# Optimization experiments

Measured on AMD Instinct MI355X. Metric: run time of the kernel, lower is better.

## Reference

```python
import jax, jax.numpy as jnp
import numpy as np

EPS = 0.001
WEIGHT = 1.0


def _grid_sample_zeros(x, grid):
    """Bilinear grid_sample, align_corners=True, zeros padding.
    x: [B,C,H,W], grid: [B,H,W,2] in [-1,1] (x then y). Returns [B,C,H,W]."""
    B, C, H, W = x.shape
    gx = (grid[..., 0] + 1.0) * 0.5 * (W - 1)  # [B,H,W] pixel coords
    gy = (grid[..., 1] + 1.0) * 0.5 * (H - 1)
    x0 = jnp.floor(gx)
    y0 = jnp.floor(gy)
    x1 = x0 + 1.0
    y1 = y0 + 1.0
    wx1 = gx - x0
    wx0 = 1.0 - wx1
    wy1 = gy - y0
    wy0 = 1.0 - wy1

    def corner(xi, yi, w):
        valid = ((xi >= 0) & (xi <= W - 1) & (yi >= 0) & (yi <= H - 1)).astype(x.dtype)
        xc = jnp.clip(xi.astype(jnp.int32), 0, W - 1)
        yc = jnp.clip(yi.astype(jnp.int32), 0, H - 1)
        vals = jax.vmap(lambda img, yy, xx: img[:, yy, xx])(x, yc, xc)  # [B,C,H,W]
        return vals * (w * valid)[:, None, :, :]

    return (corner(x0, y0, wx0 * wy0) + corner(x1, y0, wx1 * wy0)
            + corner(x0, y1, wx0 * wy1) + corner(x1, y1, wx1 * wy1))


def _warp(x, flo):
    """Warp x by flow flo (pixel units), with validity mask. x,flo: [B,*,H,W]."""
    B, C, H, W = x.shape
    xx = jnp.arange(W, dtype=x.dtype)[None, :]  # [1,W]
    yy = jnp.arange(H, dtype=x.dtype)[:, None]  # [H,1]
    grid = jnp.stack([jnp.broadcast_to(xx, (H, W)), jnp.broadcast_to(yy, (H, W))], 0)  # [2,H,W]
    vgrid = grid[None] + flo  # [B,2,H,W]
    vx = 2.0 * vgrid[:, 0] / max(W - 1, 1) - 1.0
    vy = 2.0 * vgrid[:, 1] / max(H - 1, 1) - 1.0
    vgrid_n = jnp.stack([vx, vy], -1)  # [B,H,W,2]
    out = _grid_sample_zeros(x, vgrid_n)
    ones = jnp.ones_like(x)
    mask = _grid_sample_zeros(ones, vgrid_n)
    mask = jnp.where(mask < 0.9999, 0.0, 1.0).astype(x.dtype)
    mask = jax.lax.stop_gradient(mask)  # torch writes constants in-place -> no grad
    return out * mask


def setup_inputs() -> dict:
    key = jax.random.key(0)
    k1, k2 = jax.random.split(key)
    N, H, W = 16, 768, 768
    UV_AtoB = jax.random.normal(k1, (N, 2, H, W), dtype=jnp.float32)
    UV_BtoA = jax.random.normal(k2, (N, 2, H, W), dtype=jnp.float32)
    return {"UV_AtoB": UV_AtoB, "UV_BtoA": UV_BtoA}


def reference(UV_AtoB, UV_BtoA):
    N, C, H, W = UV_AtoB.shape
    xx = jnp.broadcast_to(jnp.arange(W, dtype=jnp.float32)[None, :], (H, W))
    yy = jnp.broadcast_to(jnp.arange(H, dtype=jnp.float32)[:, None], (H, W))
    GridXY = jnp.stack([xx / max(W - 1, 1), yy / max(H - 1, 1)], 0)  # [2,H,W]
    GridXY = jnp.broadcast_to(GridXY[None], (N, 2, H, W))

    def cycle_loss(flo1, flo2):
        m = _warp(GridXY, flo1)
        m = _warp(m, flo2)
        diff = jnp.sqrt(jnp.sum((GridXY - m) ** 2, axis=1) + EPS ** 2)  # [N,H,W]
        per = jnp.sum(diff, axis=(1, 2)) / (H * W)
        return jnp.sum(per) / N

    totloss_ABA = cycle_loss(UV_AtoB, UV_BtoA)
    totloss_BAB = cycle_loss(UV_BtoA, UV_AtoB)
    return (totloss_BAB + totloss_ABA) * WEIGHT
```

## Files before the change

kernel.cpp:

```cpp
#include <hip/hip_runtime.h>

constexpr int N = 16, H = 768, W = 768;
constexpr int HW = H * W;
constexpr float EPS2 = 1.0e-6f;
constexpr float INV_W1 = 1.0f / (float)(W - 1);
constexpr float INV_H1 = 1.0f / (float)(H - 1);
constexpr float WM1 = (float)(W - 1);
constexpr float HM1 = (float)(H - 1);
constexpr float WM2 = (float)(W - 2);

constexpr int TILE_COLS = 80;
constexpr int TILE_ROWS = 24;
constexpr int C_HALO = 8;
constexpr int R_HALO = 4;
constexpr int LSTRIDE = TILE_COLS;
constexpr int TILE_FLOATS = TILE_ROWS * LSTRIDE * 2;
constexpr int NBLK_X = W / 64, NBLK_Y = H / 16;
constexpr int NBLOCKS = NBLK_X * NBLK_Y * N;

typedef float float2a __attribute__((ext_vector_type(2), aligned(4)));

struct DirMeta { float gx, gy; int xb, y0, y1; };

__device__ __forceinline__ void dir_meta(float fx, float fy, int x, int y, DirMeta& m) {
    m.gx = (float)x + fx;
    m.gy = (float)y + fy;
    float x0f = floorf(m.gx);
    float y0f = floorf(m.gy);
    m.xb = (int)fminf(fmaxf(x0f, 0.0f), WM2);
    m.y0 = (int)fminf(fmaxf(y0f, 0.0f), HM1);
    m.y1 = (int)fminf(fmaxf(y0f + 1.0f, 0.0f), HM1);
}

__device__ __forceinline__ bool fast_ok(const DirMeta& m,
                                        float2a g0, float2a g1, float2a g2, float2a g3) {
    float x0f = floorf(m.gx), y0f = floorf(m.gy);
    bool ok = (x0f >= 0.0f) & (x0f <= WM2) & (y0f >= 0.0f) & (y0f <= HM1 - 1.0f);
    float x1f = x0f + 1.0f, y1f = y0f + 1.0f;
    float gx00 = x0f + g0.x, gx01 = x1f + g0.y;
    float gx10 = x0f + g2.x, gx11 = x1f + g2.y;
    float gy00 = y0f + g1.x, gy01 = y0f + g1.y;
    float gy10 = y1f + g3.x, gy11 = y1f + g3.y;
    float xlo = fminf(fminf(gx00, gx01), fminf(gx10, gx11));
    float xhi = fmaxf(fmaxf(gx00, gx01), fmaxf(gx10, gx11));
    float ylo = fminf(fminf(gy00, gy01), fminf(gy10, gy11));
    float yhi = fmaxf(fmaxf(gy00, gy01), fmaxf(gy10, gy11));
    ok &= (xlo >= 0.0f) & (xhi <= WM1) & (ylo >= 0.0f) & (yhi <= HM1);
    return ok;
}

__device__ __forceinline__ float fast_eval(const DirMeta& m,
                                           float2a g0, float2a g1, float2a g2, float2a g3,
                                           float fxc, float fyc) {
    float x0f = floorf(m.gx), y0f = floorf(m.gy);
    float wx1 = m.gx - x0f, wy1 = m.gy - y0f;
    float ftx = fmaf(wx1, g0.y - g0.x, g0.x);
    float fbx = fmaf(wx1, g2.y - g2.x, g2.x);
    float fxv = fmaf(wy1, fbx - ftx, ftx);
    float fty = fmaf(wx1, g1.y - g1.x, g1.x);
    float fby = fmaf(wx1, g3.y - g3.x, g3.x);
    float fyv = fmaf(wy1, fby - fty, fty);
    float a = (fxc + fxv) * INV_W1;
    float b = (fyc + fyv) * INV_H1;
    return sqrtf(fmaf(a, a, fmaf(b, b, EPS2)));
}

__device__ __forceinline__ float2 wg(float fx, float fy, float xi, float yi) {
    float gx = xi + fx, gy = yi + fy;
    float x0 = floorf(gx), y0 = floorf(gy);
    float wx1 = gx - x0, wx0 = 1.0f - wx1;
    float wy1 = gy - y0, wy0 = 1.0f - wy1;
    float vx0 = (x0 >= 0.0f  && x0 <= WM1)        ? 1.0f : 0.0f;
    float vx1 = (x0 >= -1.0f && x0 <= WM1 - 1.0f) ? 1.0f : 0.0f;
    float vy0 = (y0 >= 0.0f  && y0 <= HM1)        ? 1.0f : 0.0f;
    float vy1 = (y0 >= -1.0f && y0 <= HM1 - 1.0f) ? 1.0f : 0.0f;
    float ax = wx0 * vx0, bx = wx1 * vx1, sx = ax + bx;
    float ay = wy0 * vy0, by = wy1 * vy1, sy = ay + by;
    float ms = sx * sy;
    float kx = (ms >= 0.9999f) ? INV_W1 : 0.0f;
    float ky = (ms >= 0.9999f) ? INV_H1 : 0.0f;
    float2 r;
    r.x = fmaf(sx, x0, bx) * sy * kx;
    r.y = fmaf(sy, y0, by) * sx * ky;
    return r;
}

__device__ __forceinline__ float dir_eval(const DirMeta& m,
                                          float2a r0x, float2a r0y,
                                          float2a r1x, float2a r1y,
                                          int x, int y) {
    float x0f = floorf(m.gx), y0f = floorf(m.gy);
    float wx1 = m.gx - x0f, wx0 = 1.0f - wx1;
    float wy1 = m.gy - y0f, wy0 = 1.0f - wy1;
    float x1f = x0f + 1.0f, y1f = y0f + 1.0f;
    float vx0 = (x0f >= 0.0f && x0f <= WM1) ? 1.0f : 0.0f;
    float vx1 = (x1f >= 0.0f && x1f <= WM1) ? 1.0f : 0.0f;
    float vy0 = (y0f >= 0.0f && y0f <= HM1) ? 1.0f : 0.0f;
    float vy1 = (y1f >= 0.0f && y1f <= HM1) ? 1.0f : 0.0f;
    float axw = wx0 * vx0, bxw = wx1 * vx1;
    float ayw = wy0 * vy0, byw = wy1 * vy1;
    float sxw = axw + bxw, syw = ayw + byw;
    float msum = sxw * syw;

    bool selA = (x0f >= WM1);
    bool selB = (x0f >= 0.0f);
    float fx00 = selA ? r0x.y : r0x.x;
    float fx01 = selB ? r0x.y : r0x.x;
    float fy00 = selA ? r0y.y : r0y.x;
    float fy01 = selB ? r0y.y : r0y.x;
    float fx10 = selA ? r1x.y : r1x.x;
    float fx11 = selB ? r1x.y : r1x.x;
    float fy10 = selA ? r1y.y : r1y.x;
    float fy11 = selB ? r1y.y : r1y.x;

    float x0c = fminf(fmaxf(x0f, 0.0f), WM1);
    float x1c = fminf(fmaxf(x1f, 0.0f), WM1);
    float y0c = fminf(fmaxf(y0f, 0.0f), HM1);
    float y1c = fminf(fmaxf(y1f, 0.0f), HM1);

    float2 m00 = wg(fx00, fy00, x0c, y0c);
    float2 m01 = wg(fx01, fy01, x1c, y0c);
    float2 m10 = wg(fx10, fy10, x0c, y1c);
    float2 m11 = wg(fx11, fy11, x1c, y1c);

    float w00 = axw * ayw, w10 = bxw * ayw, w01 = axw * byw, w11 = bxw * byw;
    float mx = w00 * m00.x + w10 * m01.x + w01 * m10.x + w11 * m11.x;
    float my = w00 * m00.y + w10 * m01.y + w01 * m10.y + w11 * m11.y;
    float keep = (msum >= 0.9999f) ? 1.0f : 0.0f;
    mx *= keep; my *= keep;

    float dx = (float)x * INV_W1 - mx;
    float dy = (float)y * INV_H1 - my;
    return sqrtf(fmaf(dx, dx, fmaf(dy, dy, EPS2)));
}

__device__ __forceinline__ void ld_quad(const float* t, int pix,
                                        float2a& gx, float2a& gy) {
    float2 u = *(const float2*)(t + 2 * pix);
    float2 v = *(const float2*)(t + 2 * pix + 2);
    gx.x = u.x; gx.y = v.x;
    gy.x = u.y; gy.y = v.y;
}

__global__ __launch_bounds__(256)
void cycle_loss_kernel(const float* __restrict__ A,
                       const float* __restrict__ B,
                       float* __restrict__ ws,
                       float* __restrict__ out,
                       int use_ws) {
    __shared__ float lds[2 * TILE_FLOATS];
    __shared__ float wsum[4];

    int tid  = threadIdx.x;
    int lane = tid & 63;
    int wv   = tid >> 6;
    int bx0 = blockIdx.x * 64;
    int by0 = blockIdx.y * 16;
    int b   = blockIdx.z;
    const float* Ab = A + (size_t)b * 2 * HW;
    const float* Bb = B + (size_t)b * 2 * HW;
    int tc0 = bx0 - C_HALO;
    int tr0 = by0 - R_HALO;

    for (int i = tid; i < 2 * TILE_ROWS * (TILE_COLS / 4); i += 256) {
        int t   = i / (TILE_ROWS * (TILE_COLS / 4));
        int rem = i - t * (TILE_ROWS * (TILE_COLS / 4));
        int lr  = rem / (TILE_COLS / 4);
        int lc4 = rem - lr * (TILE_COLS / 4);
        int rg = tr0 + lr;
        int cg = tc0 + lc4 * 4;
        if ((unsigned)rg < (unsigned)H && (unsigned)cg < (unsigned)W) {
            const float* src = (t ? Bb : Ab) + rg * W + cg;
            float4 fx = *(const float4*)(src);
            float4 fy = *(const float4*)(src + HW);
            float* dst = &lds[t * TILE_FLOATS + (lr * LSTRIDE + lc4 * 4) * 2];
            *(float4*)(dst)     = make_float4(fx.x, fy.x, fx.y, fy.y);
            *(float4*)(dst + 4) = make_float4(fx.z, fy.z, fx.w, fy.w);
        }
    }
    __syncthreads();

    const float* ldsA = lds;
    const float* ldsB = lds + TILE_FLOATS;
    int x  = bx0 + lane;
    int yb = by0 + wv * 4;
    int lxc = lane + C_HALO;

    float2 aC[4], bC[4];
    #pragma unroll
    for (int p = 0; p < 4; ++p) {
        int co = (wv * 4 + p + R_HALO) * LSTRIDE + lxc;
        aC[p] = *(const float2*)(ldsA + 2 * co);
        bC[p] = *(const float2*)(ldsB + 2 * co);
    }

    float s = 0.0f;
    #pragma unroll
    for (int p = 0; p < 4; ++p) {
        int y = yb + p;
        DirMeta m1, m2;
        dir_meta(bC[p].x, bC[p].y, x, y, m1);
        dir_meta(aC[p].x, aC[p].y, x, y, m2);

        bool e1 = ((unsigned)(m1.xb - tc0) <= (unsigned)(TILE_COLS - 2))
                & ((unsigned)(m1.y0 - tr0) < (unsigned)TILE_ROWS)
                & ((unsigned)(m1.y1 - tr0) < (unsigned)TILE_ROWS);
        bool e2 = ((unsigned)(m2.xb - tc0) <= (unsigned)(TILE_COLS - 2))
                & ((unsigned)(m2.y0 - tr0) < (unsigned)TILE_ROWS)
                & ((unsigned)(m2.y1 - tr0) < (unsigned)TILE_ROWS);

        float2a g1[4], g2[4];
        if (__all(e1 & e2)) {
            int i10 = (m1.y0 - tr0) * LSTRIDE + (m1.xb - tc0);
            int i11 = (m1.y1 - tr0) * LSTRIDE + (m1.xb - tc0);
            ld_quad(ldsA, i10, g1[0], g1[1]);
            ld_quad(ldsA, i11, g1[2], g1[3]);
            int i20 = (m2.y0 - tr0) * LSTRIDE + (m2.xb - tc0);
            int i21 = (m2.y1 - tr0) * LSTRIDE + (m2.xb - tc0);
            ld_quad(ldsB, i20, g2[0], g2[1]);
            ld_quad(ldsB, i21, g2[2], g2[3]);
        } else {
            if (e1) {
                int i10 = (m1.y0 - tr0) * LSTRIDE + (m1.xb - tc0);
                int i11 = (m1.y1 - tr0) * LSTRIDE + (m1.xb - tc0);
                ld_quad(ldsA, i10, g1[0], g1[1]);
                ld_quad(ldsA, i11, g1[2], g1[3]);
            } else {
                int o0 = m1.y0 * W + m1.xb, o1 = m1.y1 * W + m1.xb;
                g1[0] = *(const float2a*)(Ab + o0);
                g1[1] = *(const float2a*)(Ab + HW + o0);
                g1[2] = *(const float2a*)(Ab + o1);
                g1[3] = *(const float2a*)(Ab + HW + o1);
            }
            if (e2) {
                int i20 = (m2.y0 - tr0) * LSTRIDE + (m2.xb - tc0);
                int i21 = (m2.y1 - tr0) * LSTRIDE + (m2.xb - tc0);
                ld_quad(ldsB, i20, g2[0], g2[1]);
                ld_quad(ldsB, i21, g2[2], g2[3]);
            } else {
                int o0 = m2.y0 * W + m2.xb, o1 = m2.y1 * W + m2.xb;
                g2[0] = *(const float2a*)(Bb + o0);
                g2[1] = *(const float2a*)(Bb + HW + o0);
                g2[2] = *(const float2a*)(Bb + o1);
                g2[3] = *(const float2a*)(Bb + HW + o1);
            }
        }

        bool ok = fast_ok(m1, g1[0], g1[1], g1[2], g1[3])
                & fast_ok(m2, g2[0], g2[1], g2[2], g2[3]);
        if (__all(ok)) {
            s += fast_eval(m1, g1[0], g1[1], g1[2], g1[3], bC[p].x, bC[p].y);
            s += fast_eval(m2, g2[0], g2[1], g2[2], g2[3], aC[p].x, aC[p].y);
        } else {
            s += dir_eval(m1, g1[0], g1[1], g1[2], g1[3], x, y);
            s += dir_eval(m2, g2[0], g2[1], g2[2], g2[3], x, y);
        }
    }

    #pragma unroll
    for (int o = 32; o > 0; o >>= 1) s += __shfl_down(s, o, 64);
    if (lane == 0) wsum[wv] = s;
    __syncthreads();
    if (tid == 0) {
        float tsum = wsum[0] + wsum[1] + wsum[2] + wsum[3];
        if (use_ws) {
            int bid = (blockIdx.z * gridDim.y + blockIdx.y) * gridDim.x + blockIdx.x;
            ws[bid] = tsum;
        } else {
            atomicAdd(out, tsum * (1.0f / ((float)N * (float)H * (float)W)));
        }
    }
}

__global__ __launch_bounds__(256)
void reduce_kernel(const float* __restrict__ ws, float* __restrict__ out) {
    float s = 0.0f;
    for (int i = threadIdx.x; i < NBLOCKS; i += 256) s += ws[i];
    #pragma unroll
    for (int o = 32; o > 0; o >>= 1) s += __shfl_down(s, o, 64);
    __shared__ float wsum[4];
    int lane = threadIdx.x & 63, wv = threadIdx.x >> 6;
    if (lane == 0) wsum[wv] = s;
    __syncthreads();
    if (threadIdx.x == 0) {
        float t = wsum[0] + wsum[1] + wsum[2] + wsum[3];
        out[0] = t * (1.0f / ((float)N * (float)H * (float)W));
    }
}

extern "C" void kernel_launch(void* const* d_in, const int* in_sizes, int n_in,
                              void* d_out, int out_size, void* d_ws, size_t ws_size,
                              hipStream_t stream) {
    const float* A = (const float*)d_in[0];
    const float* B = (const float*)d_in[1];
    float* out = (float*)d_out;
    float* ws  = (float*)d_ws;

    int use_ws = (ws_size >= NBLOCKS * sizeof(float)) ? 1 : 0;
    if (!use_ws) hipMemsetAsync(out, 0, sizeof(float), stream);

    dim3 grid(NBLK_X, NBLK_Y, N);
    cycle_loss_kernel<<<grid, 256, 0, stream>>>(A, B, ws, out, use_ws);
    if (use_ws) reduce_kernel<<<1, 256, 0, stream>>>(ws, out);
}
```

Before: 209.9 us.

## Halve rows per block, shrink LDS tile, keep samples as float2 pairs

Each block now covers 8 output rows instead of 16, with each wave processing 2 rows, so the shared-memory tile drops from 24 to 17 rows. This doubles the block count, and launch bounds now request 7 blocks per SIMD. The LDS-loaded corners are kept in their interleaved (x,y) float2 form instead of being shuffled into per-channel pairs, which trims register moves, and fast_ok is rewritten with fewer ops. The trade-off is a larger halo fraction: more redundant global loads and LDS staging per output pixel, plus more blocks to schedule.

```diff
diff --git a/kernel.cpp b/kernel.cpp
--- a/kernel.cpp
+++ b/kernel.cpp
@@ -10,21 +10,21 @@
 constexpr float WM2 = (float)(W - 2);
 
 constexpr int TILE_COLS = 80;
-constexpr int TILE_ROWS = 24;
+constexpr int TILE_ROWS = 17;
 constexpr int C_HALO = 8;
 constexpr int R_HALO = 4;
 constexpr int LSTRIDE = TILE_COLS;
 constexpr int TILE_FLOATS = TILE_ROWS * LSTRIDE * 2;
-constexpr int NBLK_X = W / 64, NBLK_Y = H / 16;
+constexpr int NBLK_X = W / 64, NBLK_Y = H / 8;
 constexpr int NBLOCKS = NBLK_X * NBLK_Y * N;
 
 typedef float float2a __attribute__((ext_vector_type(2), aligned(4)));
 
 struct DirMeta { float gx, gy; int xb, y0, y1; };
 
-__device__ __forceinline__ void dir_meta(float fx, float fy, int x, int y, DirMeta& m) {
-    m.gx = (float)x + fx;
-    m.gy = (float)y + fy;
+__device__ __forceinline__ void dir_meta(float fx, float fy, float xf, float yf, DirMeta& m) {
+    m.gx = xf + fx;
+    m.gy = yf + fy;
     float x0f = floorf(m.gx);
     float y0f = floorf(m.gy);
     m.xb = (int)fminf(fmaxf(x0f, 0.0f), WM2);
@@ -33,35 +33,32 @@
 }
 
 __device__ __forceinline__ bool fast_ok(const DirMeta& m,
-                                        float2a g0, float2a g1, float2a g2, float2a g3) {
+                                        float2 u0, float2 v0, float2 u1, float2 v1) {
     float x0f = floorf(m.gx), y0f = floorf(m.gy);
-    bool ok = (x0f >= 0.0f) & (x0f <= WM2) & (y0f >= 0.0f) & (y0f <= HM1 - 1.0f);
-    float x1f = x0f + 1.0f, y1f = y0f + 1.0f;
-    float gx00 = x0f + g0.x, gx01 = x1f + g0.y;
-    float gx10 = x0f + g2.x, gx11 = x1f + g2.y;
-    float gy00 = y0f + g1.x, gy01 = y0f + g1.y;
-    float gy10 = y1f + g3.x, gy11 = y1f + g3.y;
-    float xlo = fminf(fminf(gx00, gx01), fminf(gx10, gx11));
-    float xhi = fmaxf(fmaxf(gx00, gx01), fmaxf(gx10, gx11));
-    float ylo = fminf(fminf(gy00, gy01), fminf(gy10, gy11));
-    float yhi = fmaxf(fmaxf(gy00, gy01), fmaxf(gy10, gy11));
-    ok &= (xlo >= 0.0f) & (xhi <= WM1) & (ylo >= 0.0f) & (yhi <= HM1);
-    return ok;
+    float a = v0.x + 1.0f, b = v1.x + 1.0f;
+    float xmn = fminf(fminf(u0.x, u1.x), fminf(a, b));
+    float xmx = fmaxf(fmaxf(u0.x, u1.x), fmaxf(a, b));
+    float c = u1.y + 1.0f, d = v1.y + 1.0f;
+    float ymn = fminf(fminf(u0.y, v0.y), fminf(c, d));
+    float ymx = fmaxf(fmaxf(u0.y, v0.y), fmaxf(c, d));
+    return (x0f >= 0.0f) & (x0f <= WM2) & (y0f >= 0.0f) & (y0f <= HM1 - 1.0f)
+         & (x0f + xmn >= 0.0f) & (x0f + xmx <= WM1)
+         & (y0f + ymn >= 0.0f) & (y0f + ymx <= HM1);
 }
 
 __device__ __forceinline__ float fast_eval(const DirMeta& m,
-                                           float2a g0, float2a g1, float2a g2, float2a g3,
+                                           float2 u0, float2 v0, float2 u1, float2 v1,
                                            float fxc, float fyc) {
     float x0f = floorf(m.gx), y0f = floorf(m.gy);
     float wx1 = m.gx - x0f, wy1 = m.gy - y0f;
-    float ftx = fmaf(wx1, g0.y - g0.x, g0.x);
-    float fbx = fmaf(wx1, g2.y - g2.x, g2.x);
-    float fxv = fmaf(wy1, fbx - ftx, ftx);
-    float fty = fmaf(wx1, g1.y - g1.x, g1.x);
-    float fby = fmaf(wx1, g3.y - g3.x, g3.x);
-    float fyv = fmaf(wy1, fby - fty, fty);
-    float a = (fxc + fxv) * INV_W1;
-    float b = (fyc + fyv) * INV_H1;
+    float ftx = fmaf(wx1, v0.x - u0.x, u0.x);
+    float fty = fmaf(wx1, v0.y - u0.y, u0.y);
+    float fbx = fmaf(wx1, v1.x - u1.x, u1.x);
+    float fby = fmaf(wx1, v1.y - u1.y, u1.y);
+    float fvx = fmaf(wy1, fbx - ftx, ftx);
+    float fvy = fmaf(wy1, fby - fty, fty);
+    float a = (fxc + fvx) * INV_W1;
+    float b = (fyc + fvy) * INV_H1;
     return sqrtf(fmaf(a, a, fmaf(b, b, EPS2)));
 }
 
@@ -86,8 +83,7 @@
 }
 
 __device__ __forceinline__ float dir_eval(const DirMeta& m,
-                                          float2a r0x, float2a r0y,
-                                          float2a r1x, float2a r1y,
+                                          float2 u0, float2 v0, float2 u1, float2 v1,
                                           int x, int y) {
     float x0f = floorf(m.gx), y0f = floorf(m.gy);
     float wx1 = m.gx - x0f, wx0 = 1.0f - wx1;
@@ -104,14 +100,14 @@
 
     bool selA = (x0f >= WM1);
     bool selB = (x0f >= 0.0f);
-    float fx00 = selA ? r0x.y : r0x.x;
-    float fx01 = selB ? r0x.y : r0x.x;
-    float fy00 = selA ? r0y.y : r0y.x;
-    float fy01 = selB ? r0y.y : r0y.x;
-    float fx10 = selA ? r1x.y : r1x.x;
-    float fx11 = selB ? r1x.y : r1x.x;
-    float fy10 = selA ? r1y.y : r1y.x;
-    float fy11 = selB ? r1y.y : r1y.x;
+    float fx00 = selA ? v0.x : u0.x;
+    float fx01 = selB ? v0.x : u0.x;
+    float fy00 = selA ? v0.y : u0.y;
+    float fy01 = selB ? v0.y : u0.y;
+    float fx10 = selA ? v1.x : u1.x;
+    float fx11 = selB ? v1.x : u1.x;
+    float fy10 = selA ? v1.y : u1.y;
+    float fy11 = selB ? v1.y : u1.y;
 
     float x0c = fminf(fmaxf(x0f, 0.0f), WM1);
     float x1c = fminf(fmaxf(x1f, 0.0f), WM1);
@@ -134,15 +130,12 @@
     return sqrtf(fmaf(dx, dx, fmaf(dy, dy, EPS2)));
 }
 
-__device__ __forceinline__ void ld_quad(const float* t, int pix,
-                                        float2a& gx, float2a& gy) {
-    float2 u = *(const float2*)(t + 2 * pix);
-    float2 v = *(const float2*)(t + 2 * pix + 2);
-    gx.x = u.x; gx.y = v.x;
-    gy.x = u.y; gy.y = v.y;
-}
-
-__global__ __launch_bounds__(256)
+__device__ __forceinline__ void ld_quad(const float* t, int pix, float2& u, float2& v) {
+    u = *(const float2*)(t + 2 * pix);
+    v = *(const float2*)(t + 2 * pix + 2);
+}
+
+__global__ __launch_bounds__(256, 7)
 void cycle_loss_kernel(const float* __restrict__ A,
                        const float* __restrict__ B,
                        float* __restrict__ ws,
@@ -155,18 +148,20 @@
     int lane = tid & 63;
     int wv   = tid >> 6;
     int bx0 = blockIdx.x * 64;
-    int by0 = blockIdx.y * 16;
+    int by0 = blockIdx.y * 8;
     int b   = blockIdx.z;
     const float* Ab = A + (size_t)b * 2 * HW;
     const float* Bb = B + (size_t)b * 2 * HW;
     int tc0 = bx0 - C_HALO;
     int tr0 = by0 - R_HALO;
 
-    for (int i = tid; i < 2 * TILE_ROWS * (TILE_COLS / 4); i += 256) {
-        int t   = i / (TILE_ROWS * (TILE_COLS / 4));
-        int rem = i - t * (TILE_ROWS * (TILE_COLS / 4));
-        int lr  = rem / (TILE_COLS / 4);
-        int lc4 = rem - lr * (TILE_COLS / 4);
+    constexpr int ROW_CHUNKS = TILE_COLS / 4;
+    constexpr int TASKS_PER_T = TILE_ROWS * ROW_CHUNKS;
+    for (int i = tid; i < 2 * TASKS_PER_T; i += 256) {
+        int t   = i / TASKS_PER_T;
+        int rem = i - t * TASKS_PER_T;
+        int lr  = rem / ROW_CHUNKS;
+        int lc4 = rem - lr * ROW_CHUNKS;
         int rg = tr0 + lr;
         int cg = tc0 + lc4 * 4;
         if ((unsigned)rg < (unsigned)H && (unsigned)cg < (unsigned)W) {
@@ -183,77 +178,77 @@
     const float* ldsA = lds;
     const float* ldsB = lds + TILE_FLOATS;
     int x  = bx0 + lane;
-    int yb = by0 + wv * 4;
+    int yb = by0 + wv * 2;
     int lxc = lane + C_HALO;
-
-    float2 aC[4], bC[4];
+    float xf = (float)x;
+
+    float2 aC[2], bC[2];
     #pragma unroll
-    for (int p = 0; p < 4; ++p) {
-        int co = (wv * 4 + p + R_HALO) * LSTRIDE + lxc;
+    for (int p = 0; p < 2; ++p) {
+        int co = (wv * 2 + p + R_HALO) * LSTRIDE + lxc;
         aC[p] = *(const float2*)(ldsA + 2 * co);
         bC[p] = *(const float2*)(ldsB + 2 * co);
     }
 
     float s = 0.0f;
     #pragma unroll
-    for (int p = 0; p < 4; ++p) {
+    for (int p = 0; p < 2; ++p) {
         int y = yb + p;
+        float yf = (float)y;
         DirMeta m1, m2;
-        dir_meta(bC[p].x, bC[p].y, x, y, m1);
-        dir_meta(aC[p].x, aC[p].y, x, y, m2);
-
-        bool e1 = ((unsigned)(m1.xb - tc0) <= (unsigned)(TILE_COLS - 2))
-                & ((unsigned)(m1.y0 - tr0) < (unsigned)TILE_ROWS)
-                & ((unsigned)(m1.y1 - tr0) < (unsigned)TILE_ROWS);
-        bool e2 = ((unsigned)(m2.xb - tc0) <= (unsigned)(TILE_COLS - 2))
-                & ((unsigned)(m2.y0 - tr0) < (unsigned)TILE_ROWS)
-                & ((unsigned)(m2.y1 - tr0) < (unsigned)TILE_ROWS);
-
-        float2a g1[4], g2[4];
+        dir_meta(bC[p].x, bC[p].y, xf, yf, m1);
+        dir_meta(aC[p].x, aC[p].y, xf, yf, m2);
+
+        int x1l = m1.xb - tc0, y1l0 = m1.y0 - tr0, y1l1 = m1.y1 - tr0;
+        int x2l = m2.xb - tc0, y2l0 = m2.y0 - tr0, y2l1 = m2.y1 - tr0;
+        bool e1 = ((unsigned)x1l <= (unsigned)(TILE_COLS - 2))
+                & ((unsigned)y1l0 < (unsigned)TILE_ROWS)
+                & ((unsigned)y1l1 < (unsigned)TILE_ROWS);
+        bool e2 = ((unsigned)x2l <= (unsigned)(TILE_COLS - 2))
+                & ((unsigned)y2l0 < (unsigned)TILE_ROWS)
+                & ((unsigned)y2l1 < (unsigned)TILE_ROWS);
+
+        float2 u10, v10, u11, v11, u20, v20, u21, v21;
         if (__all(e1 & e2)) {
-            int i10 = (m1.y0 - tr0) * LSTRIDE + (m1.xb - tc0);
-            int i11 = (m1.y1 - tr0) * LSTRIDE + (m1.xb - tc0);
-            ld_quad(ldsA, i10, g1[0], g1[1]);
-            ld_quad(ldsA, i11, g1[2], g1[3]);
-            int i20 = (m2.y0 - tr0) * LSTRIDE + (m2.xb - tc0);
-            int i21 = (m2.y1 - tr0) * LSTRIDE + (m2.xb - tc0);
-            ld_quad(ldsB, i20, g2[0], g2[1]);
-            ld_quad(ldsB, i21, g2[2], g2[3]);
+            ld_quad(ldsA, y1l0 * LSTRIDE + x1l, u10, v10);
+            ld_quad(ldsA, y1l1 * LSTRIDE + x1l, u11, v11);
+            ld_quad(ldsB, y2l0 * LSTRIDE + x2l, u20, v20);
+            ld_quad(ldsB, y2l1 * LSTRIDE + x2l, u21, v21);
         } else {
             if (e1) {
-                int i10 = (m1.y0 - tr0) * LSTRIDE + (m1.xb - tc0);
-                int i11 = (m1.y1 - tr0) * LSTRIDE + (m1.xb - tc0);
-                ld_quad(ldsA, i10, g1[0], g1[1]);
-                ld_quad(ldsA, i11, g1[2], g1[3]);
+                ld_quad(ldsA, y1l0 * LSTRIDE + x1l, u10, v10);
+                ld_quad(ldsA, y1l1 * LSTRIDE + x1l, u11, v11);
             } else {
                 int o0 = m1.y0 * W + m1.xb, o1 = m1.y1 * W + m1.xb;
-                g1[0] = *(const float2a*)(Ab + o0);
-                g1[1] = *(const float2a*)(Ab + HW + o0);
-                g1[2] = *(const float2a*)(Ab + o1);
-                g1[3] = *(const float2a*)(Ab + HW + o1);
+                float2a rx0 = *(const float2a*)(Ab + o0);
+                float2a ry0 = *(const float2a*)(Ab + HW + o0);
+                float2a rx1 = *(const float2a*)(Ab + o1);
+                float2a ry1 = *(const float2a*)(Ab + HW + o1);
+                u10 = make_float2(rx0.x, ry0.x); v10 = make_float2(rx0.y, ry0.y);
+                u11 = make_float2(rx1.x, ry1.x); v11 = make_float2(rx1.y, ry1.y);
             }
             if (e2) {
-                int i20 = (m2.y0 - tr0) * LSTRIDE + (m2.xb - tc0);
-                int i21 = (m2.y1 - tr0) * LSTRIDE + (m2.xb - tc0);
-                ld_quad(ldsB, i20, g2[0], g2[1]);
-                ld_quad(ldsB, i21, g2[2], g2[3]);
+                ld_quad(ldsB, y2l0 * LSTRIDE + x2l, u20, v20);
+                ld_quad(ldsB, y2l1 * LSTRIDE + x2l, u21, v21);
             } else {
                 int o0 = m2.y0 * W + m2.xb, o1 = m2.y1 * W + m2.xb;
-                g2[0] = *(const float2a*)(Bb + o0);
-                g2[1] = *(const float2a*)(Bb + HW + o0);
-                g2[2] = *(const float2a*)(Bb + o1);
-                g2[3] = *(const float2a*)(Bb + HW + o1);
+                float2a rx0 = *(const float2a*)(Bb + o0);
+                float2a ry0 = *(const float2a*)(Bb + HW + o0);
+                float2a rx1 = *(const float2a*)(Bb + o1);
+                float2a ry1 = *(const float2a*)(Bb + HW + o1);
+                u20 = make_float2(rx0.x, ry0.x); v20 = make_float2(rx0.y, ry0.y);
+                u21 = make_float2(rx1.x, ry1.x); v21 = make_float2(rx1.y, ry1.y);
             }
         }
 
-        bool ok = fast_ok(m1, g1[0], g1[1], g1[2], g1[3])
-                & fast_ok(m2, g2[0], g2[1], g2[2], g2[3]);
+        bool ok = fast_ok(m1, u10, v10, u11, v11)
+                & fast_ok(m2, u20, v20, u21, v21);
         if (__all(ok)) {
-            s += fast_eval(m1, g1[0], g1[1], g1[2], g1[3], bC[p].x, bC[p].y);
-            s += fast_eval(m2, g2[0], g2[1], g2[2], g2[3], aC[p].x, aC[p].y);
+            s += fast_eval(m1, u10, v10, u11, v11, bC[p].x, bC[p].y);
+            s += fast_eval(m2, u20, v20, u21, v21, aC[p].x, aC[p].y);
         } else {
-            s += dir_eval(m1, g1[0], g1[1], g1[2], g1[3], x, y);
-            s += dir_eval(m2, g2[0], g2[1], g2[2], g2[3], x, y);
+            s += dir_eval(m1, u10, v10, u11, v11, x, y);
+            s += dir_eval(m2, u20, v20, u21, v21, x, y);
         }
     }
 
```

Result: slower. 224.3 us (+6.9%).
